# Kernel tuning notes

Hardware: AMD Instinct MI355X
Metric: run time of the kernel (lower is better)

The kernel has to match this reference:

```python
import jax, jax.numpy as jnp
import numpy as np

B, S, H = 2, 1024, 4096
NH, NKV, D = 32, 8, 128
N_REP = NH // NKV
SCALE = D ** -0.5
ROPE_BASE = 1000000.0
NEG_INF = -1e9


def _rope_tables(dtype=jnp.float32):
    inv_freq = 1.0 / (ROPE_BASE ** (jnp.arange(0, D, 2, dtype=jnp.float32) / D))
    pos = jnp.arange(S, dtype=jnp.float32)
    freqs = pos[:, None] * inv_freq[None, :]              # [S, D/2]
    emb = jnp.concatenate([freqs, freqs], axis=-1)        # [S, D]
    cos = jnp.broadcast_to(jnp.cos(emb)[None], (B, S, D)).astype(dtype)
    sin = jnp.broadcast_to(jnp.sin(emb)[None], (B, S, D)).astype(dtype)
    return cos, sin


def setup_inputs() -> dict:
    key = jax.random.key(0)
    k1, k2, k3, k4, k5 = jax.random.split(key, 5)
    hidden_states = jax.random.normal(k1, (B, S, H), dtype=jnp.float32)
    # weights stored as [in, out] so application is x @ W
    Wq = jax.random.normal(k2, (H, NH * D), dtype=jnp.float32) * (H ** -0.5)
    Wk = jax.random.normal(k3, (H, NKV * D), dtype=jnp.float32) * (H ** -0.5)
    Wv = jax.random.normal(k4, (H, NKV * D), dtype=jnp.float32) * (H ** -0.5)
    Wo = jax.random.normal(k5, (NH * D, H), dtype=jnp.float32) * ((NH * D) ** -0.5)
    cos, sin = _rope_tables()
    causal = jnp.tril(jnp.ones((S, S), dtype=bool))
    attention_mask = jnp.where(causal, 0.0, NEG_INF).astype(jnp.float32)
    attention_mask = jnp.broadcast_to(attention_mask[None, None], (B, 1, S, S))
    return {"hidden_states": hidden_states, "cos": cos, "sin": sin,
            "attention_mask": attention_mask, "Wq": Wq, "Wk": Wk, "Wv": Wv, "Wo": Wo}


def _rotate_half(x):
    x1, x2 = x[..., : D // 2], x[..., D // 2:]
    return jnp.concatenate([-x2, x1], axis=-1)


def reference(hidden_states, cos, sin, attention_mask, Wq, Wk, Wv, Wo):
    # projections -> [B, heads, S, D]
    q = (hidden_states @ Wq).reshape(B, S, NH, D).transpose(0, 2, 1, 3)
    k = (hidden_states @ Wk).reshape(B, S, NKV, D).transpose(0, 2, 1, 3)
    v = (hidden_states @ Wv).reshape(B, S, NKV, D).transpose(0, 2, 1, 3)
    # RoPE (cos/sin unsqueezed over head dim)
    c = cos[:, None, :, :]
    s = sin[:, None, :, :]
    q = q * c + _rotate_half(q) * s
    k = k * c + _rotate_half(k) * s
    # repeat_kv for GQA
    k = jnp.repeat(k, N_REP, axis=1)   # [B, NH, S, D]
    v = jnp.repeat(v, N_REP, axis=1)
    scores = jnp.einsum('bhqd,bhkd->bhqk', q, k) * SCALE + attention_mask
    weights = jax.nn.softmax(scores.astype(jnp.float32), axis=-1).astype(q.dtype)
    attn = jnp.einsum('bhqk,bhkd->bhqd', weights, v)
    attn = attn.transpose(0, 2, 1, 3).reshape(B, S, NH * D)
    return attn @ Wo
```

## Files before the change

kernel.cpp:

```cpp
#include <hip/hip_runtime.h>

typedef unsigned short u16;
typedef __bf16 bf16x8 __attribute__((ext_vector_type(8)));
typedef float f32x4 __attribute__((ext_vector_type(4)));

#define SCALE_QK 0.08838834764831845f
#define LOG2E 1.4426950408889634f
#define NEGBIG (-1e9f)

static __device__ __forceinline__ float bf2f(u16 u) {
  union { float f; unsigned int i; } x; x.i = ((unsigned int)u) << 16; return x.f;
}
static __device__ __forceinline__ u16 f2bf(float f) {
  union { float f; unsigned int i; } x; x.f = f;
  return (u16)((x.i + 0x7fffu + ((x.i >> 16) & 1u)) >> 16);
}
static __device__ __forceinline__ void async16(const u16* g, u16* s) {
  __builtin_amdgcn_global_load_lds(
      (const __attribute__((address_space(1))) void*)g,
      (__attribute__((address_space(3))) void*)s, 16, 0, 0);
}

__global__ __launch_bounds__(64) void detect_dtype(
    const void* p0, const void* p1, const void* p2, const void* p3,
    const void* p4, const void* p5, int* flags) {
  const void* ps[6] = {p0, p1, p2, p3, p4, p5};
  const u16* p = (const u16*)ps[blockIdx.x];
  int lane = threadIdx.x;
  u16 u = p[2 * lane];
  int e = (u >> 7) & 0xFF;
  int plaus = (e >= 112 && e <= 143) ? 1 : 0;
  unsigned long long m = __ballot(plaus);
  if (lane == 0) {
    flags[blockIdx.x] = (__popcll(m) < 32) ? 1 : 0;
    if (blockIdx.x == 0) flags[6] = 0;
  }
}

static __device__ __forceinline__ void transpose_body(
    const void* __restrict__ src, u16* __restrict__ dst, int N, int K,
    int n0, int k0, int f32in, u16* t) {
  const int LT = 74;
  const int tid = threadIdx.x;
  for (int c = tid; c < 512; c += 256) {
    int r = c >> 3, ch = (c & 7) * 8;
    u16* tp = t + r * LT + ch;
    if (f32in) {
      const float* p = (const float*)src + (size_t)(k0 + r) * N + n0 + ch;
      float4 v0 = *(const float4*)p;
      float4 v1 = *(const float4*)(p + 4);
      tp[0] = f2bf(v0.x); tp[1] = f2bf(v0.y); tp[2] = f2bf(v0.z); tp[3] = f2bf(v0.w);
      tp[4] = f2bf(v1.x); tp[5] = f2bf(v1.y); tp[6] = f2bf(v1.z); tp[7] = f2bf(v1.w);
    } else {
      uint4 v = *(const uint4*)((const u16*)src + (size_t)(k0 + r) * N + n0 + ch);
      const u16* pv = (const u16*)&v;
#pragma unroll
      for (int e = 0; e < 8; ++e) tp[e] = pv[e];
    }
  }
  __syncthreads();
  for (int c = tid; c < 512; c += 256) {
    int rr = c >> 3, cc = (c & 7) * 8;
    u16 tmp[8];
#pragma unroll
    for (int e = 0; e < 8; ++e) tmp[e] = t[(cc + e) * LT + rr];
    *(uint4*)(dst + (size_t)(n0 + rr) * K + k0 + cc) = *(const uint4*)tmp;
  }
}

__global__ __launch_bounds__(256) void transpose_to_bf16(
    const void* __restrict__ src, u16* __restrict__ dst, int N, int K,
    const int* __restrict__ flag) {
  __shared__ u16 t[64 * 74];
  transpose_body(src, dst, N, K, blockIdx.x * 64, blockIdx.y * 64, *flag, t);
}

__global__ __launch_bounds__(256) void prep_fused(
    const void* __restrict__ Wq, const void* __restrict__ Wk,
    const void* __restrict__ Wv, u16* __restrict__ dst,
    const void* __restrict__ hidden, u16* __restrict__ Xb,
    const int* __restrict__ flags) {
  __shared__ u16 t[64 * 74];
  int bx = blockIdx.x;
  if (bx < 96) {
    const void* src; u16* d; int N; int f32in; int nx;
    if (bx < 64)      { src = Wq; d = dst;                       N = 4096; f32in = flags[2]; nx = bx; }
    else if (bx < 80) { src = Wk; d = dst + (size_t)4096 * 4096; N = 1024; f32in = flags[3]; nx = bx - 64; }
    else              { src = Wv; d = dst + (size_t)5120 * 4096; N = 1024; f32in = flags[4]; nx = bx - 80; }
    transpose_body(src, d, N, 4096, nx * 64, blockIdx.y * 64, f32in, t);
  } else {
    int i = (((bx - 96) * 64 + blockIdx.y) * 256 + threadIdx.x) * 8;
    if (flags[0]) {
      float4 v0 = *(const float4*)((const float*)hidden + i);
      float4 v1 = *(const float4*)((const float*)hidden + i + 4);
      u16 tmp[8] = {f2bf(v0.x), f2bf(v0.y), f2bf(v0.z), f2bf(v0.w),
                    f2bf(v1.x), f2bf(v1.y), f2bf(v1.z), f2bf(v1.w)};
      *(uint4*)(Xb + i) = *(const uint4*)tmp;
    } else {
      *(uint4*)(Xb + i) = *(const uint4*)((const u16*)hidden + i);
    }
  }
}

template <int BM, int BN, int NWM, int NWN>
__global__ __launch_bounds__(512, 2) void gemm_8ph(
    const u16* __restrict__ A, const u16* __restrict__ Bt, void* __restrict__ C,
    int K, int lda, int ldb, int ldc, const int* __restrict__ oflag) {
  constexpr int WM = BM / NWM, WN = BN / NWN;
  constexpr int FM = WM / 16, FN = WN / 16;
  constexpr int FMH = FM / 2, FNH = FN / 2;
  constexpr int BHALF = BN / 2;
  constexpr int AU = 128 * 64;
  constexpr int BU = BHALF * 64;
  constexpr int BLD = BU / (512 * 8);
  __shared__ u16 lds[(AU + BU) * 4];
  const int tid = threadIdx.x;
  const int wave = tid >> 6, lane = tid & 63;
  const int quad = lane >> 4, l16 = lane & 15;
  const int wr = wave / NWN, wc = wave % NWN;

  const int nwg = gridDim.x * gridDim.y;
  const int flat = blockIdx.y * gridDim.x + blockIdx.x;
  const int swz = (flat & 7) * (nwg >> 3) + (flat >> 3);
  const int bm = (swz % gridDim.y) * BM;
  const int bn = (swz / gridDim.y) * BN;
  const int f32out = *oflag;
  const int NK = K >> 6;

  constexpr int UO[8] = {0, AU, AU + BU, AU + 2 * BU,
                         2 * AU + 2 * BU, 3 * AU + 2 * BU,
                         3 * AU + 3 * BU, 3 * AU + 4 * BU};

  const int arow0 = wr * WM;
  const int brow0 = wc * WN;

  auto stage = [&](int u, int kt) {
    if (kt >= NK) return;
    u16* base = lds + UO[u];
    int us = u & 3;
    if (us == 0 || us == 3) {
      int mh = (us == 3);
#pragma unroll
      for (int c0 = 0; c0 < 2; ++c0) {
        int c = c0 * 512 + tid;
        int row = bm + mh * 128 + (c >> 3);
        int col = kt * 64 + ((c & 7) ^ ((c >> 3) & 7)) * 8;
        async16(A + (size_t)row * lda + col, base + c * 8);
      }
    } else {
      int nh = (us == 2);
#pragma unroll
      for (int c0 = 0; c0 < BLD; ++c0) {
        int c = c0 * 512 + tid;
        int row = bn + nh * BHALF + (c >> 3);
        int col = kt * 64 + ((c & 7) ^ ((c >> 3) & 7)) * 8;
        async16(Bt + (size_t)row * ldb + col, base + c * 8);
      }
    }
  };

  f32x4 acc[FM][FN] = {};
  bf16x8 af[FMH][2];
  bf16x8 bvh[2][FNH][2];

  stage(0, 0); stage(1, 0); stage(2, 0); stage(3, 0);
  stage(5, 1); stage(6, 1);
  if constexpr (BLD == 2) { asm volatile("s_waitcnt vmcnt(4)" ::: "memory"); }
  else                    { asm volatile("s_waitcnt vmcnt(2)" ::: "memory"); }
  asm volatile("s_barrier" ::: "memory");

  constexpr int SU[8]  = {4, 7, 1, 2, 0, 3, 5, 6};
  constexpr int SKT[8] = {1, 1, 2, 2, 2, 2, 3, 3};

  const int IT = NK >> 1;
#pragma unroll 1
  for (int it = 0; it < IT; ++it) {
#pragma unroll
    for (int p = 0; p < 8; ++p) {
      const int kt = p >> 2, sub = p & 3;
      const int mh = sub >> 1, nh = sub & 1;
      if (sub == 0 || sub == 2) {
        const int r0 = arow0 + mh * (WM / 2);
        const u16* abase = lds + UO[kt * 4 + ((r0 >> 7) ? 3 : 0)];
        const int lr0 = r0 & 127;
#pragma unroll
        for (int mi = 0; mi < FMH; ++mi) {
          const int lr = lr0 + mi * 16 + l16;
#pragma unroll
          for (int ks = 0; ks < 2; ++ks)
            af[mi][ks] = *(const bf16x8*)(
                abase + lr * 64 + (((ks * 4 + quad) ^ (lr & 7)) * 8));
        }
      }
      if (sub == 0 || sub == 1) {
        const int c0 = brow0 + nh * FNH * 16;
        const u16* bbase = lds + UO[kt * 4 + 1 + (c0 / BHALF)];
        const int lc0 = c0 % BHALF;
#pragma unroll
        for (int ni = 0; ni < FNH; ++ni) {
          const int lr = lc0 + ni * 16 + l16;
#pragma unroll
          for (int ks = 0; ks < 2; ++ks)
            bvh[nh][ni][ks] = *(const bf16x8*)(
                bbase + lr * 64 + (((ks * 4 + quad) ^ (lr & 7)) * 8));
        }
      }
      stage(SU[p], 2 * it + SKT[p]);
      if (sub == 0 && FM == 8)
        asm volatile("s_waitcnt lgkmcnt(8)" ::: "memory");
      asm volatile("s_barrier" ::: "memory");
      asm volatile("s_waitcnt lgkmcnt(0)" ::: "memory");
      __builtin_amdgcn_sched_barrier(0);
      __builtin_amdgcn_s_setprio(1);
#pragma unroll
      for (int mi = 0; mi < FMH; ++mi)
#pragma unroll
        for (int ni = 0; ni < FNH; ++ni) {
          f32x4* a = &acc[mh * FMH + mi][nh * FNH + ni];
          *a = __builtin_amdgcn_mfma_f32_16x16x32_bf16(af[mi][0], bvh[nh][ni][0], *a, 0, 0, 0);
          *a = __builtin_amdgcn_mfma_f32_16x16x32_bf16(af[mi][1], bvh[nh][ni][1], *a, 0, 0, 0);
        }
      __builtin_amdgcn_s_setprio(0);
      if (p == 3 || p == 7) {
        if constexpr (BLD == 2) { asm volatile("s_waitcnt vmcnt(4)" ::: "memory"); }
        else                    { asm volatile("s_waitcnt vmcnt(2)" ::: "memory"); }
      }
      asm volatile("s_barrier" ::: "memory");
    }
  }

#pragma unroll
  for (int mi = 0; mi < FM; ++mi) {
    int row = bm + wr * WM + mi * 16 + quad * 4;
#pragma unroll
    for (int ni = 0; ni < FN; ++ni) {
      int col = bn + wc * WN + ni * 16 + l16;
#pragma unroll
      for (int r = 0; r < 4; ++r) {
        size_t idx = (size_t)(row + r) * ldc + col;
        if (f32out) ((float*)C)[idx] = acc[mi][ni][r];
        else ((u16*)C)[idx] = f2bf(acc[mi][ni][r]);
      }
    }
  }
}

__global__ __launch_bounds__(256) void rope_kernel(
    u16* __restrict__ QKV, const void* __restrict__ cosb,
    const void* __restrict__ sinb, const int* __restrict__ flag) {
  int idx = blockIdx.x * 256 + threadIdx.x;
  int d8 = (idx & 7) * 8;
  int rest = idx >> 3;
  int slot = rest % 40;
  int tok = rest / 40;
  int col = (slot < 32) ? (slot * 128 + d8) : (4096 + (slot - 32) * 128 + d8);
  size_t base = (size_t)tok * 6144 + col;
  uint4 va = *(const uint4*)(QKV + base);
  uint4 vb = *(const uint4*)(QKV + base + 64);
  const u16* pa = (const u16*)&va;
  const u16* pb = (const u16*)&vb;
  size_t cb = (size_t)tok * 128 + d8;
  float c1[8], s1[8], c2[8], s2[8];
  if (*flag) {
    const float* cp = (const float*)cosb + cb;
    const float* sp = (const float*)sinb + cb;
    float4 t0 = *(const float4*)cp,        t1 = *(const float4*)(cp + 4);
    float4 t2 = *(const float4*)(cp + 64), t3 = *(const float4*)(cp + 68);
    float4 u0 = *(const float4*)sp,        u1 = *(const float4*)(sp + 4);
    float4 u2 = *(const float4*)(sp + 64), u3 = *(const float4*)(sp + 68);
    c1[0]=t0.x;c1[1]=t0.y;c1[2]=t0.z;c1[3]=t0.w;c1[4]=t1.x;c1[5]=t1.y;c1[6]=t1.z;c1[7]=t1.w;
    c2[0]=t2.x;c2[1]=t2.y;c2[2]=t2.z;c2[3]=t2.w;c2[4]=t3.x;c2[5]=t3.y;c2[6]=t3.z;c2[7]=t3.w;
    s1[0]=u0.x;s1[1]=u0.y;s1[2]=u0.z;s1[3]=u0.w;s1[4]=u1.x;s1[5]=u1.y;s1[6]=u1.z;s1[7]=u1.w;
    s2[0]=u2.x;s2[1]=u2.y;s2[2]=u2.z;s2[3]=u2.w;s2[4]=u3.x;s2[5]=u3.y;s2[6]=u3.z;s2[7]=u3.w;
  } else {
    const u16* cp = (const u16*)cosb + cb;
    const u16* sp = (const u16*)sinb + cb;
    uint4 t0 = *(const uint4*)cp, t1 = *(const uint4*)(cp + 64);
    uint4 u0 = *(const uint4*)sp, u1 = *(const uint4*)(sp + 64);
    const u16* q0 = (const u16*)&t0; const u16* q1 = (const u16*)&t1;
    const u16* r0 = (const u16*)&u0; const u16* r1 = (const u16*)&u1;
#pragma unroll
    for (int e = 0; e < 8; ++e) {
      c1[e] = bf2f(q0[e]); c2[e] = bf2f(q1[e]);
      s1[e] = bf2f(r0[e]); s2[e] = bf2f(r1[e]);
    }
  }
  u16 o1[8], o2[8];
#pragma unroll
  for (int e = 0; e < 8; ++e) {
    float x1 = bf2f(pa[e]), x2 = bf2f(pb[e]);
    o1[e] = f2bf(x1 * c1[e] - x2 * s1[e]);
    o2[e] = f2bf(x2 * c2[e] + x1 * s2[e]);
  }
  *(uint4*)(QKV + base) = *(const uint4*)o1;
  *(uint4*)(QKV + base + 64) = *(const uint4*)o2;
}

__global__ __launch_bounds__(256, 3) void attn_kernel(
    const u16* __restrict__ QKV, u16* __restrict__ O) {
  const int LK = 136;
  const int LP = 72;
  __shared__ u16 sK[64 * LK];
  __shared__ u16 sV[128 * 64];
  __shared__ u16 sP[64 * LP];
  const int tid = threadIdx.x, wave = tid >> 6, lane = tid & 63;
  const int quad = lane >> 4, l16 = lane & 15;
  const int pp = blockIdx.x, h = blockIdx.y, b = blockIdx.z;
  const int kvh = h >> 2;
  const size_t tb = (size_t)b * 1024 * 6144;
  const u16* Qg = QKV + tb + (size_t)h * 128;
  const u16* Kg = QKV + tb + 4096 + (size_t)kvh * 128;
  const u16* Vg = QKV + tb + 5120 + (size_t)kvh * 128;

#pragma unroll 1
  for (int pass = 0; pass < 2; ++pass) {
    const int qt = pass ? (15 - pp) : pp;

    bf16x8 qa[4];
    {
      const int qrow = qt * 64 + wave * 16 + l16;
#pragma unroll
      for (int kc = 0; kc < 4; ++kc) {
        bf16x8 v = *(const bf16x8*)(Qg + (size_t)qrow * 6144 + kc * 32 + quad * 8);
#pragma unroll
        for (int e = 0; e < 8; ++e) v[e] = (__bf16)((float)v[e] * (SCALE_QK * LOG2E));
        qa[kc] = v;
      }
    }

    uint4 kreg[4], vreg[4];
#pragma unroll
    for (int i = 0; i < 4; ++i) {
      int c = i * 256 + tid, row = c >> 4, ch = (c & 15) * 8;
      kreg[i] = *(const uint4*)(Kg + (size_t)row * 6144 + ch);
      vreg[i] = *(const uint4*)(Vg + (size_t)row * 6144 + ch);
    }

    float m_run = -INFINITY, l_run = 0.f;
    f32x4 oacc[8] = {};
    const int qg = qt * 64 + wave * 16 + l16;

    const int nkb = qt + 1;
    for (int kb = 0; kb < nkb; ++kb) {
#pragma unroll
      for (int i = 0; i < 4; ++i) {
        int c = i * 256 + tid, row = c >> 4, ch = (c & 15) * 8;
        *(uint4*)(sK + row * LK + ch) = kreg[i];
        const u16* pw = (const u16*)&vreg[i];
#pragma unroll
        for (int e = 0; e < 8; ++e) {
          int d = ch + e;
          sV[d * 64 + ((((row >> 3) ^ (d >> 3)) & 7) << 3) + (row & 7)] = pw[e];
        }
      }
      __syncthreads();
      if (kb + 1 < nkb) {
#pragma unroll
        for (int i = 0; i < 4; ++i) {
          int c = i * 256 + tid, row = c >> 4, ch = (c & 15) * 8;
          kreg[i] = *(const uint4*)(Kg + (size_t)((kb + 1) * 64 + row) * 6144 + ch);
          vreg[i] = *(const uint4*)(Vg + (size_t)((kb + 1) * 64 + row) * 6144 + ch);
        }
      }

      f32x4 st[4] = {};
#pragma unroll
      for (int kc = 0; kc < 4; ++kc)
#pragma unroll
        for (int j = 0; j < 4; ++j) {
          bf16x8 bb = *(const bf16x8*)(sK + (j * 16 + l16) * LK + kc * 32 + quad * 8);
          st[j] = __builtin_amdgcn_mfma_f32_16x16x32_bf16(bb, qa[kc], st[j], 0, 0, 0);
        }

      const int kg0 = kb * 64 + quad * 4;
      float mloc = NEGBIG;
#pragma unroll
      for (int j = 0; j < 4; ++j)
#pragma unroll
        for (int r = 0; r < 4; ++r) {
          float v = st[j][r];
          if (kg0 + j * 16 + r > qg) v = NEGBIG;
          st[j][r] = v;
          mloc = fmaxf(mloc, v);
        }
      mloc = fmaxf(mloc, __shfl_xor(mloc, 16, 64));
      mloc = fmaxf(mloc, __shfl_xor(mloc, 32, 64));

      if (__any(mloc - m_run > 8.0f)) {
        float mn = fmaxf(m_run, mloc);
        float alpha = exp2f(m_run - mn);
        m_run = mn;
        l_run *= alpha;
        float ar[4];
#pragma unroll
        for (int r = 0; r < 4; ++r) ar[r] = __shfl(alpha, quad * 4 + r, 64);
#pragma unroll
        for (int dt = 0; dt < 8; ++dt)
#pragma unroll
          for (int r = 0; r < 4; ++r) oacc[dt][r] *= ar[r];
      }

      float lad = 0.f;
#pragma unroll
      for (int j = 0; j < 4; ++j)
#pragma unroll
        for (int r = 0; r < 4; ++r) {
          float p = exp2f(st[j][r] - m_run);
          st[j][r] = p;
          lad += p;
        }
      lad += __shfl_xor(lad, 16, 64);
      lad += __shfl_xor(lad, 32, 64);
      l_run += lad;

#pragma unroll
      for (int j = 0; j < 4; ++j)
#pragma unroll
        for (int r = 0; r < 4; ++r)
          sP[(wave * 16 + l16) * LP + j * 16 + quad * 4 + r] = f2bf(st[j][r]);
      __asm__ __volatile__("s_waitcnt lgkmcnt(0)" ::: "memory");

#pragma unroll
      for (int kc = 0; kc < 2; ++kc) {
        bf16x8 a = *(const bf16x8*)(sP + (wave * 16 + l16) * LP + kc * 32 + quad * 8);
#pragma unroll
        for (int dt = 0; dt < 8; ++dt) {
          int d = dt * 16 + l16;
          int chk = ((kc * 4 + quad) ^ (d >> 3)) & 7;
          bf16x8 bb = *(const bf16x8*)(sV + d * 64 + chk * 8);
          oacc[dt] = __builtin_amdgcn_mfma_f32_16x16x32_bf16(a, bb, oacc[dt], 0, 0, 0);
        }
      }
      __syncthreads();
    }

    float lfin[4];
#pragma unroll
    for (int r = 0; r < 4; ++r) lfin[r] = __shfl(l_run, quad * 4 + r, 64);

    const int srow = qt * 64 + wave * 16 + quad * 4;
#pragma unroll
    for (int dt = 0; dt < 8; ++dt)
#pragma unroll
      for (int r = 0; r < 4; ++r) {
        float val = oacc[dt][r] / lfin[r];
        O[((size_t)b * 1024 + srow + r) * 4096 + h * 128 + dt * 16 + l16] = f2bf(val);
      }
  }
}

extern "C" void kernel_launch(void* const* d_in, const int* in_sizes, int n_in,
                              void* d_out, int out_size, void* d_ws, size_t ws_size,
                              hipStream_t stream) {
  (void)in_sizes; (void)n_in; (void)out_size; (void)ws_size;
  const void* hidden = d_in[0];
  const void* cosb   = d_in[1];
  const void* sinb   = d_in[2];
  const void* Wq = d_in[4];
  const void* Wk = d_in[5];
  const void* Wv = d_in[6];
  const void* Wo = d_in[7];

  u16* ws = (u16*)d_ws;
  u16* Wqkvt = ws;
  u16* Wot   = ws;
  u16* Xb    = ws + (size_t)25165824;
  u16* attnb = Xb;
  u16* QKV   = ws + (size_t)33554432;
  int* flags = (int*)(ws + (size_t)46137344);

  detect_dtype<<<6, 64, 0, stream>>>(hidden, cosb, Wq, Wk, Wv, Wo, flags);

  prep_fused<<<dim3(160, 64), 256, 0, stream>>>(Wq, Wk, Wv, Wqkvt, hidden, Xb, flags);

  gemm_8ph<256, 256, 2, 4><<<dim3(24, 8), 512, 0, stream>>>(
      Xb, Wqkvt, QKV, 4096, 4096, 4096, 6144, flags + 6);
  rope_kernel<<<2560, 256, 0, stream>>>(QKV, cosb, sinb, flags + 1);

  transpose_to_bf16<<<dim3(64, 64), 256, 0, stream>>>(Wo, Wot, 4096, 4096, flags + 5);

  attn_kernel<<<dim3(8, 32, 2), 256, 0, stream>>>(QKV, attnb);

  gemm_8ph<256, 128, 4, 2><<<dim3(32, 8), 512, 0, stream>>>(
      attnb, Wot, d_out, 4096, 4096, 4096, 4096, flags + 0);
}
```

Baseline: 483.7 us.

## Rebalance causal attention tiles across 11 blocks and add 4-phase output GEMM

The attention grid goes from 8 to 11 blocks per head. Block g always handles query tile 15-g, and blocks 6-10 also take a second short tile, g-6. This changes how the causal work is paired, with more workgroups and different load balance. The output projection now uses a new gemm_4ph kernel with a 256x128 tile, double-buffered async LDS staging split into A and B halves, and launch bounds (512,2). That should allow two workgroups per CU and change overlap compared with the 8-phase kernel. The risk is more LDS pressure, and the waitcnt accounting being wrong at the tail.

Measured after the change: 481.5 us. No clear change (-0.5%).

```diff
diff --git a/kernel.cpp b/kernel.cpp
--- a/kernel.cpp
+++ b/kernel.cpp
@@ -130,7 +130,6 @@
   constexpr int UO[8] = {0, AU, AU + BU, AU + 2 * BU,
                          2 * AU + 2 * BU, 3 * AU + 2 * BU,
                          3 * AU + 3 * BU, 3 * AU + 4 * BU};
-
   const int arow0 = wr * WM;
   const int brow0 = wc * WN;
 
@@ -235,6 +234,126 @@
 #pragma unroll
     for (int ni = 0; ni < FN; ++ni) {
       int col = bn + wc * WN + ni * 16 + l16;
+#pragma unroll
+      for (int r = 0; r < 4; ++r) {
+        size_t idx = (size_t)(row + r) * ldc + col;
+        if (f32out) ((float*)C)[idx] = acc[mi][ni][r];
+        else ((u16*)C)[idx] = f2bf(acc[mi][ni][r]);
+      }
+    }
+  }
+}
+
+__global__ __launch_bounds__(512, 2) void gemm_4ph(
+    const u16* __restrict__ A, const u16* __restrict__ Bt, void* __restrict__ C,
+    int K, int lda, int ldb, int ldc, const int* __restrict__ oflag) {
+  constexpr int AU = 128 * 64;
+  constexpr int BH = 64 * 64;
+  __shared__ u16 lds[2 * (2 * AU + 2 * BH)];
+  const int tid = threadIdx.x;
+  const int wave = tid >> 6, lane = tid & 63;
+  const int quad = lane >> 4, l16 = lane & 15;
+  const int wr = wave >> 1, wc = wave & 1;
+
+  const int nwg = gridDim.x * gridDim.y;
+  const int flat = blockIdx.y * gridDim.x + blockIdx.x;
+  const int swz = (flat & 7) * (nwg >> 3) + (flat >> 3);
+  const int bm = (swz % gridDim.y) * 256;
+  const int bn = (swz / gridDim.y) * 128;
+  const int f32out = *oflag;
+  const int NK = K >> 6;
+
+  auto stageA = [&](int par, int half, int kt) {
+    if (kt >= NK) return;
+    u16* base = lds + par * 24576 + half * 8192;
+#pragma unroll
+    for (int c0 = 0; c0 < 2; ++c0) {
+      int c = c0 * 512 + tid;
+      int row = bm + half * 128 + (c >> 3);
+      int col = kt * 64 + ((c & 7) ^ ((c >> 3) & 7)) * 8;
+      async16(A + (size_t)row * lda + col, base + c * 8);
+    }
+  };
+  auto stageB = [&](int par, int half, int kt) {
+    if (kt >= NK) return;
+    u16* base = lds + par * 24576 + 16384 + half * 4096;
+    int c = tid;
+    int row = bn + half * 64 + (c >> 3);
+    int col = kt * 64 + ((c & 7) ^ ((c >> 3) & 7)) * 8;
+    async16(Bt + (size_t)row * ldb + col, base + c * 8);
+  };
+
+  f32x4 acc[4][4] = {};
+  bf16x8 af[2][2], bv[4][2];
+
+  stageA(0, 0, 0); stageA(0, 1, 0); stageB(0, 0, 0); stageB(0, 1, 0);
+  stageB(1, 0, 1); stageB(1, 1, 1);
+  asm volatile("s_waitcnt vmcnt(2)" ::: "memory");
+  asm volatile("s_barrier" ::: "memory");
+
+  const int IT = NK >> 1;
+#pragma unroll 1
+  for (int it = 0; it < IT; ++it) {
+#pragma unroll
+    for (int p = 0; p < 4; ++p) {
+      const int par = p >> 1, mh = p & 1;
+      const u16* abase = lds + par * 24576 + (wr >> 1) * 8192;
+      const int lr0 = (wr & 1) * 64 + mh * 32;
+#pragma unroll
+      for (int mi = 0; mi < 2; ++mi) {
+        const int lr = lr0 + mi * 16 + l16;
+#pragma unroll
+        for (int ks = 0; ks < 2; ++ks)
+          af[mi][ks] = *(const bf16x8*)(
+              abase + lr * 64 + (((ks * 4 + quad) ^ (lr & 7)) * 8));
+      }
+      if (mh == 0) {
+        const u16* bbase = lds + par * 24576 + 16384 + wc * 4096;
+#pragma unroll
+        for (int ni = 0; ni < 4; ++ni) {
+          const int lr = ni * 16 + l16;
+#pragma unroll
+          for (int ks = 0; ks < 2; ++ks)
+            bv[ni][ks] = *(const bf16x8*)(
+                bbase + lr * 64 + (((ks * 4 + quad) ^ (lr & 7)) * 8));
+        }
+      }
+      if (p == 0)      { stageA(1, 0, 2 * it + 1); stageA(1, 1, 2 * it + 1); }
+      else if (p == 1) { stageB(0, 0, 2 * it + 2); stageB(0, 1, 2 * it + 2); }
+      else if (p == 2) { stageA(0, 0, 2 * it + 2); stageA(0, 1, 2 * it + 2); }
+      else             { stageB(1, 0, 2 * it + 3); stageB(1, 1, 2 * it + 3); }
+      if (mh == 0)
+        asm volatile("s_waitcnt lgkmcnt(8)" ::: "memory");
+      asm volatile("s_barrier" ::: "memory");
+      asm volatile("s_waitcnt lgkmcnt(0)" ::: "memory");
+      __builtin_amdgcn_sched_barrier(0);
+      __builtin_amdgcn_s_setprio(1);
+#pragma unroll
+      for (int mi = 0; mi < 2; ++mi)
+#pragma unroll
+        for (int ni = 0; ni < 4; ++ni) {
+          f32x4* a = &acc[mh * 2 + mi][ni];
+          *a = __builtin_amdgcn_mfma_f32_16x16x32_bf16(af[mi][0], bv[ni][0], *a, 0, 0, 0);
+          *a = __builtin_amdgcn_mfma_f32_16x16x32_bf16(af[mi][1], bv[ni][1], *a, 0, 0, 0);
+        }
+      __builtin_amdgcn_s_setprio(0);
+      if (p == 1) {
+        if (2 * it + 2 < NK) { asm volatile("s_waitcnt vmcnt(2)" ::: "memory"); }
+        else                 { asm volatile("s_waitcnt vmcnt(0)" ::: "memory"); }
+      } else if (p == 3) {
+        if (2 * it + 3 < NK) { asm volatile("s_waitcnt vmcnt(2)" ::: "memory"); }
+        else                 { asm volatile("s_waitcnt vmcnt(0)" ::: "memory"); }
+      }
+      asm volatile("s_barrier" ::: "memory");
+    }
+  }
+
+#pragma unroll
+  for (int mi = 0; mi < 4; ++mi) {
+    int row = bm + wr * 64 + mi * 16 + quad * 4;
+#pragma unroll
+    for (int ni = 0; ni < 4; ++ni) {
+      int col = bn + wc * 64 + ni * 16 + l16;
 #pragma unroll
       for (int r = 0; r < 4; ++r) {
         size_t idx = (size_t)(row + r) * ldc + col;
@@ -305,7 +424,9 @@
   __shared__ u16 sP[64 * LP];
   const int tid = threadIdx.x, wave = tid >> 6, lane = tid & 63;
   const int quad = lane >> 4, l16 = lane & 15;
-  const int pp = blockIdx.x, h = blockIdx.y, b = blockIdx.z;
+  const int g = blockIdx.x, h = blockIdx.y, b = blockIdx.z;
+  const int qtA = 15 - g;
+  const int qtB = (g >= 6) ? (g - 6) : -1;
   const int kvh = h >> 2;
   const size_t tb = (size_t)b * 1024 * 6144;
   const u16* Qg = QKV + tb + (size_t)h * 128;
@@ -314,7 +435,8 @@
 
 #pragma unroll 1
   for (int pass = 0; pass < 2; ++pass) {
-    const int qt = pass ? (15 - pp) : pp;
+    const int qt = pass ? qtB : qtA;
+    if (qt < 0) break;
 
     bf16x8 qa[4];
     {
@@ -479,8 +601,8 @@
 
   transpose_to_bf16<<<dim3(64, 64), 256, 0, stream>>>(Wo, Wot, 4096, 4096, flags + 5);
 
-  attn_kernel<<<dim3(8, 32, 2), 256, 0, stream>>>(QKV, attnb);
-
-  gemm_8ph<256, 128, 4, 2><<<dim3(32, 8), 512, 0, stream>>>(
+  attn_kernel<<<dim3(11, 32, 2), 256, 0, stream>>>(QKV, attnb);
+
+  gemm_4ph<<<dim3(32, 8), 512, 0, stream>>>(
       attnb, Wot, d_out, 4096, 4096, 4096, 4096, flags + 0);
 }
```
